# Kernel tuning notes

Measured on AMD Instinct MI355X. Metric: run time of the kernel, lower is better.

The kernel has to match this reference:

```python
import jax, jax.numpy as jnp
import numpy as np

EDGES = np.array([[0,13],[0,1],[0,4],[0,10],[0,7],[13,14],[14,15],[15,16],[1,2],[2,3],
                  [3,17],[4,5],[5,6],[6,18],[10,11],[11,12],[12,19],[7,8],[8,9],[9,20]])
N = 21
EPS = 1e-5


def _build_adj():
    # adj_mx_from_edges: symmetric binary adjacency + self-loops, row-normalized (D^-1 (A+I))
    A = np.zeros((N, N), np.float32)
    A[EDGES[:, 0], EDGES[:, 1]] = 1.0
    A = np.maximum(A, A.T)
    A = A + np.eye(N, dtype=np.float32)
    A = A / A.sum(1, keepdims=True)
    return A


def setup_inputs() -> dict:
    key = jax.random.key(0)
    ks = jax.random.split(key, 10)
    B, C, H, W = 64, 256, 64, 64
    s = 0.05
    return {
        "feature_s": jax.random.normal(ks[0], (B, C, H, W), jnp.float32),
        "target_s": jax.random.uniform(ks[1], (B, N, H, W), jnp.float32),
        "adj": jnp.asarray(_build_adj()),
        "bn_gamma": jnp.ones((N,), jnp.float32),
        "bn_beta": jnp.zeros((N,), jnp.float32),
        "gru_wx": s * jax.random.normal(ks[2], (256, 768), jnp.float32),
        "gru_wh": s * jax.random.normal(ks[3], (256, 768), jnp.float32),
        "gru_bx": jnp.zeros((768,), jnp.float32),
        "gru_bh": jnp.zeros((768,), jnp.float32),
        "w_g1": s * jax.random.normal(ks[4], (2, 256, 256), jnp.float32),
        "b_g1": jnp.zeros((256,), jnp.float32),
        "w_g2": s * jax.random.normal(ks[5], (2, 256, 256), jnp.float32),
        "b_g2": jnp.zeros((256,), jnp.float32),
        "w_out": s * jax.random.normal(ks[6], (2, 256, 3), jnp.float32),
        "b_out": jnp.zeros((3,), jnp.float32),
    }


def _batchnorm1d(x, gamma, beta):
    # x: [B, 21, C]; BatchNorm1d over channel dim 21 (stats over batch and length)
    mean = jnp.mean(x, axis=(0, 2), keepdims=True)
    var = jnp.var(x, axis=(0, 2), keepdims=True)
    xn = (x - mean) * jax.lax.rsqrt(var + EPS)
    return xn * gamma[None, :, None] + beta[None, :, None]


def _gru(x, wx, wh, bx, bh):
    # standard GRU scanned over the 21-joint axis; x: [B, N, 256] -> [B, N, 256]
    B, n, Hd = x.shape
    xg = jnp.einsum('bnc,ch->bnh', x, wx) + bx  # [B, N, 3H]

    def step(h, xg_t):
        hg = h @ wh + bh
        r = jax.nn.sigmoid(xg_t[..., :Hd] + hg[..., :Hd])
        z = jax.nn.sigmoid(xg_t[..., Hd:2 * Hd] + hg[..., Hd:2 * Hd])
        ncand = jnp.tanh(xg_t[..., 2 * Hd:] + r * hg[..., 2 * Hd:])
        h_new = (1.0 - z) * ncand + z * h
        return h_new, h_new

    h0 = jnp.zeros((B, Hd), x.dtype)
    _, ys = jax.lax.scan(step, h0, jnp.swapaxes(xg, 0, 1))
    return jnp.swapaxes(ys, 0, 1)


def _laplacian(adj):
    # normalized Laplacian L = I - D^{-1/2} A D^{-1/2}
    d = adj.sum(-1)
    dinv = jnp.where(d > 0, jax.lax.rsqrt(jnp.where(d > 0, d, 1.0)), 0.0)
    return jnp.eye(N, dtype=adj.dtype) - dinv[:, None] * adj * dinv[None, :]


def _chebconv(x, L, w, b):
    # K=2 Chebyshev conv: T0 = I, T1 = L ->  x @ W0 + (L x) @ W1 + b
    return jnp.einsum('bnc,co->bno', x, w[0]) + jnp.einsum('nm,bmc,co->bno', L, x, w[1]) + b


def reference(feature_s, target_s, adj, bn_gamma, bn_beta,
              gru_wx, gru_wh, gru_bx, gru_bh,
              w_g1, b_g1, w_g2, b_g2, w_out, b_out):
    B, C, H, W = feature_s.shape
    # batched correlation: [B, 21, HW] x [B, HW, C] -> [B, 21, C]
    q = jnp.einsum('bjp,bcp->bjc',
                   target_s.reshape(B, N, H * W),
                   feature_s.reshape(B, C, H * W))
    q = _batchnorm1d(q, bn_gamma, bn_beta)
    q = jnp.where(q > 0, q, 0.1 * q)  # LeakyReLU(0.1)
    q = _gru(q, gru_wx, gru_wh, gru_bx, gru_bh)
    # _ResChebGC: two graph convs with ReLU + residual (dropout = identity in eval)
    L = _laplacian(adj)
    h = jax.nn.relu(_chebconv(q, L, w_g1, b_g1))
    h = jax.nn.relu(_chebconv(h, L, w_g2, b_g2))
    x = q + h
    return _chebconv(x, L, w_out, b_out)  # [B, 21, 3]
```

## Files before the change

### kernel.cpp

```cpp
#include <hip/hip_runtime.h>
#include <cstdint>

#define B   64
#define NJ  21
#define CHN 256
#define HW  4096
#define G3  768
#define KSTEP 64

typedef _Float16 f16x8 __attribute__((ext_vector_type(8)));
typedef float    f32x4 __attribute__((ext_vector_type(4)));
typedef _Float16 f16x2 __attribute__((ext_vector_type(2)));
typedef __fp16   fp16x2v __attribute__((ext_vector_type(2)));
union PKU { fp16x2v h; unsigned u; };
union HU { unsigned u; f16x2 h; };

static __device__ inline unsigned pack_f16(float a, float b){
  HU u; u.h.x = (_Float16)a; u.h.y = (_Float16)b; return u.u;
}

__global__ __launch_bounds__(64) void k_lap(const float* __restrict__ adj, float* __restrict__ L){
  __shared__ float dinv[NJ];
  int t = threadIdx.x;
  if (t < NJ){
    float s = 0.f;
    for (int j=0;j<NJ;j++) s += adj[t*NJ+j];
    dinv[t] = s > 0.f ? 1.f/sqrtf(s) : 0.f;
  }
  __syncthreads();
  for (int idx=t; idx<NJ*NJ; idx+=64){
    int i = idx/NJ, j = idx%NJ;
    L[idx] = (i==j ? 1.f : 0.f) - dinv[i]*adj[idx]*dinv[j];
  }
}

__global__ __launch_bounds__(256,2) void k_corr2(const float* __restrict__ T,
    const float* __restrict__ F, _Float16* __restrict__ P){
  int bid = blockIdx.x;
  int nb = bid & 3, b = (bid>>2)&63, kb = bid>>8;
  int t = threadIdx.x;
  int w = t>>6, l = t&63;
  __shared__ __align__(16) unsigned short At[2][32*KSTEP];
  __shared__ __align__(16) unsigned short Bt[2][64*KSTEP];

  for (int i=t; i<704; i+=256){
    int bi = (i>=352) ? 1 : 0; int r2 = i - bi*352;
    int r = 21 + (r2>>5); int kk = r2 & 31;
    *(unsigned*)((char*)&At[bi][0] + r*128 + kk*4) = 0u;
  }

  bool isF = (t < 128);
  bool isT = (t >= 128) && (t < 170);
  const float4* gp = nullptr; int srow = 0, shalf = 0;
  if (isF){
    srow = t>>1; shalf = t&1;
    gp = (const float4*)(F + ((size_t)b*CHN + nb*64 + srow)*HW + (size_t)kb*2048) + shalf*8;
  } else if (isT){
    int tt = t-128; srow = tt>>1; shalf = tt&1;
    gp = (const float4*)(T + ((size_t)b*NJ + srow)*HW + (size_t)kb*2048) + shalf*8;
  }
  float4 ld[8];
  if (gp){
    #pragma unroll
    for (int i=0;i<8;i++) ld[i] = gp[i];
  }

  f32x4 acc0 = {0.f,0.f,0.f,0.f}, acc1 = {0.f,0.f,0.f,0.f};
  int arow0 = (l&15);
  int brow  = w*16 + (l&15);
  int kbyt  = (l>>4)*16;

  for (int s=0; s<32; ++s){
    int bi = s & 1;
    if (gp){
      unsigned short* tile = isF ? &Bt[bi][0] : &At[bi][0];
      #pragma unroll
      for (int i=0;i<8;i++){
        PKU p0, p1;
        p0.h = __builtin_amdgcn_cvt_pkrtz(ld[i].x, ld[i].y);
        p1.h = __builtin_amdgcn_cvt_pkrtz(ld[i].z, ld[i].w);
        int addr = (srow*128 + shalf*64 + i*8) ^ ((srow&7)<<4);
        uint2 v; v.x = p0.u; v.y = p1.u;
        *(uint2*)((char*)tile + addr) = v;
      }
      if (s < 31){
        const float4* gn = gp + (size_t)(s+1)*16;
        #pragma unroll
        for (int i=0;i<8;i++) ld[i] = gn[i];
      }
    }
    __syncthreads();
    #pragma unroll
    for (int kc=0;kc<2;kc++){
      int kb2 = kc*64 + kbyt;
      int ab0 = ((arow0)*128      + kb2) ^ ((arow0&7)<<4);
      int ab1 = ((arow0+16)*128   + kb2) ^ ((arow0&7)<<4);
      int bb  = ((brow)*128       + kb2) ^ ((brow&7)<<4);
      f16x8 a0 = *(const f16x8*)((const char*)&At[bi][0] + ab0);
      f16x8 a1 = *(const f16x8*)((const char*)&At[bi][0] + ab1);
      f16x8 bf = *(const f16x8*)((const char*)&Bt[bi][0] + bb);
      acc0 = __builtin_amdgcn_mfma_f32_16x16x32_f16(a0, bf, acc0, 0, 0, 0);
      acc1 = __builtin_amdgcn_mfma_f32_16x16x32_f16(a1, bf, acc1, 0, 0, 0);
    }
    __syncthreads();
  }

  int cbase = nb*64 + w*16 + (l&15);
  #pragma unroll
  for (int r=0;r<4;r++){
    int row0 = (l>>4)*4 + r;
    if (row0 < 21)
      P[(((size_t)kb*64 + b)*21 + row0)*256 + cbase] = (_Float16)acc0[r];
    int row1 = row0 + 16;
    if (row1 < 21)
      P[(((size_t)kb*64 + b)*21 + row1)*256 + cbase] = (_Float16)acc1[r];
  }
}

__global__ __launch_bounds__(256) void k_stats(const _Float16* __restrict__ P,
    float* __restrict__ q, float* __restrict__ stats){
  int j = blockIdx.x, t = threadIdx.x;
  float s = 0.f, ss = 0.f;
  for (int b=0;b<B;b++){
    size_t i0 = ((size_t)b*21 + j)*256 + t;
    float v = (float)P[i0] + (float)P[(size_t)64*21*256 + i0];
    q[((size_t)b*NJ + j)*CHN + t] = v;
    s += v; ss += v*v;
  }
  #pragma unroll
  for (int o=32;o>0;o>>=1){ s += __shfl_down(s,o); ss += __shfl_down(ss,o); }
  __shared__ float sb[4], ssb[4];
  int wid = t>>6;
  if ((t&63)==0){ sb[wid]=s; ssb[wid]=ss; }
  __syncthreads();
  if (t==0){
    float S  = sb[0]+sb[1]+sb[2]+sb[3];
    float SS = ssb[0]+ssb[1]+ssb[2]+ssb[3];
    float mean = S * (1.f/16384.f);
    float var  = SS * (1.f/16384.f) - mean*mean;
    stats[j]      = mean;
    stats[NJ + j] = 1.f/sqrtf(var + 1e-5f);
  }
}

__global__ __launch_bounds__(256) void k_xg(const float* __restrict__ q,
    const float* __restrict__ stats, const float* __restrict__ gamma, const float* __restrict__ beta,
    const float* __restrict__ wx, const float* __restrict__ bx, float* __restrict__ xg){
  int b = blockIdx.x/3, sl = blockIdx.x%3;
  int t = threadIdx.x;
  int col = sl*256 + t;
  __shared__ float xn[NJ][CHN];
  for (int idx=t; idx<NJ*CHN; idx+=256){
    int j = idx >> 8;
    float v = (q[(size_t)b*NJ*CHN + idx] - stats[j]) * stats[NJ+j];
    v = v * gamma[j] + beta[j];
    xn[j][idx & 255] = v > 0.f ? v : 0.1f*v;
  }
  __syncthreads();
  float acc[NJ];
  #pragma unroll
  for (int j=0;j<NJ;j++) acc[j]=0.f;
  for (int c=0;c<CHN;c++){
    float wv = wx[(size_t)c*G3 + col];
    #pragma unroll
    for (int j=0;j<NJ;j++) acc[j] += xn[j][c]*wv;
  }
  float bv = bx[col];
  #pragma unroll
  for (int j=0;j<NJ;j++) xg[((size_t)b*NJ+j)*G3 + col] = acc[j] + bv;
}

__global__ __launch_bounds__(256) void k_pack(const float* __restrict__ wh, unsigned* __restrict__ whp){
  int idx = blockIdx.x*256 + threadIdx.x;
  int c2 = idx / G3, col = idx % G3;
  float w0 = wh[(size_t)(2*c2)*G3 + col];
  float w1 = wh[(size_t)(2*c2+1)*G3 + col];
  whp[idx] = pack_f16(w0, w1);
}

__global__ __launch_bounds__(768,3) void k_gru(const unsigned* __restrict__ whp,
    const float* __restrict__ bh, const float* __restrict__ xg, float* __restrict__ gout){
  int b = blockIdx.x;
  int col = threadIdx.x;
  int l = col & 63;
  __shared__ float hf[256];
  __shared__ float lr[256], lz[256];
  float bhv = bh[col];
  if (col < 256) hf[col] = 0.f;
  unsigned hv0 = 0u, hv1 = 0u;
  float xv_next = xg[((size_t)b*NJ + 0)*G3 + col];
  __syncthreads();
  for (int step=0; step<NJ; ++step){
    float xvc = xv_next;
    if (step < NJ-1) xv_next = xg[((size_t)b*NJ + step+1)*G3 + col];
    float a0 = 0.f, a1 = 0.f;
    #pragma unroll
    for (int c2=0; c2<64; ++c2){
      HU w; w.u = whp[c2*G3 + col];
      HU h; h.u = __builtin_amdgcn_readlane(hv0, c2);
#if __has_builtin(__builtin_amdgcn_fdot2)
      a0 = __builtin_amdgcn_fdot2(w.h, h.h, a0, false);
#else
      a0 += (float)w.h.x*(float)h.h.x + (float)w.h.y*(float)h.h.y;
#endif
    }
    #pragma unroll
    for (int c2=0; c2<64; ++c2){
      HU w; w.u = whp[(64+c2)*G3 + col];
      HU h; h.u = __builtin_amdgcn_readlane(hv1, c2);
#if __has_builtin(__builtin_amdgcn_fdot2)
      a1 = __builtin_amdgcn_fdot2(w.h, h.h, a1, false);
#else
      a1 += (float)w.h.x*(float)h.h.x + (float)w.h.y*(float)h.h.y;
#endif
    }
    float a = a0 + a1 + bhv;
    if (col < 256)      lr[col]     = 1.f/(1.f+__expf(-(xvc + a)));
    else if (col < 512) lz[col-256] = 1.f/(1.f+__expf(-(xvc + a)));
    __syncthreads();
    if (col >= 512){
      int i = col - 512;
      float nv = tanhf(xvc + lr[i]*a);
      float z  = lz[i];
      float hnew = (1.f - z)*nv + z*hf[i];
      gout[((size_t)b*NJ + step)*CHN + i] = hnew;
      hf[i] = hnew;
    }
    __syncthreads();
    float2 p0 = *(const float2*)&hf[2*l];
    float2 p1 = *(const float2*)&hf[128 + 2*l];
    hv0 = pack_f16(p0.x, p0.y);
    hv1 = pack_f16(p1.x, p1.y);
  }
}

__global__ __launch_bounds__(256) void k_cheb(const float* __restrict__ xin,
    const float* __restrict__ Lm, const float* __restrict__ W,
    const float* __restrict__ bvec, float* __restrict__ out){
  int b = blockIdx.x >> 2, oq = blockIdx.x & 3;
  int t = threadIdx.x;
  int ol = t & 63, ck = t >> 6;
  __shared__ float xs[NJ][CHN];
  __shared__ float lx[NJ][CHN];
  __shared__ float part[4][64][NJ];
  for (int idx=t; idx<NJ*CHN; idx+=256) xs[idx>>8][idx&255] = xin[(size_t)b*NJ*CHN + idx];
  __syncthreads();
  for (int idx=t; idx<NJ*CHN; idx+=256){
    int j = idx>>8, c = idx&255;
    float sacc = 0.f;
    #pragma unroll
    for (int m=0;m<NJ;m++) sacc += Lm[j*NJ+m]*xs[m][c];
    lx[j][c] = sacc;
  }
  __syncthreads();
  int o = oq*64 + ol;
  float acc[NJ];
  #pragma unroll
  for (int j=0;j<NJ;j++) acc[j]=0.f;
  const float* W0 = W;
  const float* W1 = W + CHN*CHN;
  for (int cc=0; cc<64; ++cc){
    int c = ck*64 + cc;
    float w0 = W0[(size_t)c*CHN + o];
    float w1 = W1[(size_t)c*CHN + o];
    #pragma unroll
    for (int j=0;j<NJ;j++){ acc[j] += xs[j][c]*w0; acc[j] += lx[j][c]*w1; }
  }
  #pragma unroll
  for (int j=0;j<NJ;j++) part[ck][ol][j] = acc[j];
  __syncthreads();
  for (int idx=t; idx<64*NJ; idx+=256){
    int o2 = idx & 63, j = idx >> 6;
    float s2 = part[0][o2][j]+part[1][o2][j]+part[2][o2][j]+part[3][o2][j] + bvec[oq*64+o2];
    s2 = s2 > 0.f ? s2 : 0.f;
    out[(size_t)b*NJ*CHN + j*CHN + oq*64 + o2] = s2;
  }
}

__global__ __launch_bounds__(64) void k_out(const float* __restrict__ gq, const float* __restrict__ h2,
    const float* __restrict__ Lm, const float* __restrict__ W, const float* __restrict__ bvec,
    float* __restrict__ out){
  int b = blockIdx.x, t = threadIdx.x;
  __shared__ float xs[NJ][CHN];
  __shared__ float lx[NJ][CHN];
  for (int idx=t; idx<NJ*CHN; idx+=64)
    xs[idx>>8][idx&255] = gq[(size_t)b*NJ*CHN+idx] + h2[(size_t)b*NJ*CHN+idx];
  __syncthreads();
  for (int idx=t; idx<NJ*CHN; idx+=64){
    int j = idx>>8, c = idx&255;
    float s = 0.f;
    #pragma unroll
    for (int m=0;m<NJ;m++) s += Lm[j*NJ+m]*xs[m][c];
    lx[j][c] = s;
  }
  __syncthreads();
  if (t < 63){
    int j = t/3, o = t%3;
    float acc = bvec[o];
    const float* W0 = W;
    const float* W1 = W + CHN*3;
    for (int c=0;c<CHN;c++){
      acc += xs[j][c]*W0[c*3+o];
      acc += lx[j][c]*W1[c*3+o];
    }
    out[(size_t)b*63 + t] = acc;
  }
}

extern "C" void kernel_launch(void* const* d_in, const int* in_sizes, int n_in,
                              void* d_out, int out_size, void* d_ws, size_t ws_size,
                              hipStream_t stream){
  const float* feat  = (const float*)d_in[0];
  const float* targ  = (const float*)d_in[1];
  const float* adj   = (const float*)d_in[2];
  const float* gamma = (const float*)d_in[3];
  const float* beta  = (const float*)d_in[4];
  const float* wx    = (const float*)d_in[5];
  const float* wh    = (const float*)d_in[6];
  const float* bx    = (const float*)d_in[7];
  const float* bh    = (const float*)d_in[8];
  const float* wg1   = (const float*)d_in[9];
  const float* bg1   = (const float*)d_in[10];
  const float* wg2   = (const float*)d_in[11];
  const float* bg2   = (const float*)d_in[12];
  const float* wout  = (const float*)d_in[13];
  const float* bout  = (const float*)d_in[14];

  float* ws   = (float*)d_ws;
  float* q     = ws + 0;
  float* stats = ws + 344064;
  float* Lw    = ws + 344128;
  float* xgw   = ws + 344576;
  float* gout  = ws + 1376768;
  float* h1    = ws + 1720832;
  float* h2b   = ws + 2064896;
  _Float16* P = (_Float16*)(ws + 344576);
  unsigned* whp = (unsigned*)h1;

  k_lap  <<<1,    64, 0, stream>>>(adj, Lw);
  k_pack <<<384, 256, 0, stream>>>(wh, whp);
  k_corr2<<<512, 256, 0, stream>>>(targ, feat, P);
  k_stats<<<21,  256, 0, stream>>>(P, q, stats);
  k_xg   <<<192, 256, 0, stream>>>(q, stats, gamma, beta, wx, bx, xgw);
  k_gru  <<<64,  768, 0, stream>>>(whp, bh, xgw, gout);
  k_cheb <<<256, 256, 0, stream>>>(gout, Lw, wg1, bg1, h1);
  k_cheb <<<256, 256, 0, stream>>>(h1,   Lw, wg2, bg2, h2b);
  k_out  <<<64,   64, 0, stream>>>(gout, h2b, Lw, wout, bout, (float*)d_out);
}
```

Measured before the change: 262.1 us.

## Split correlation K four ways, cache GRU weights in registers, trim barriers

The correlation kernel now splits the 4096-long reduction into four chunks over 1024 blocks instead of two chunks over 512, to raise occupancy. It stores tiles with 16-byte LDS writes and uses one barrier per step instead of two. The stats kernel sums four partials. The GRU recurrent weights are repacked per column so each thread keeps its 128 packed weights in registers across all 21 steps instead of reloading them from global memory each step. That register cost may cause spills or limit occupancy, and dropping the trailing barrier relies on double buffering to avoid races.

Measured after the change: 280.2 us. 6.9% more time.

```diff
diff --git a/kernel.cpp b/kernel.cpp
--- a/kernel.cpp
+++ b/kernel.cpp
@@ -6,7 +6,6 @@
 #define CHN 256
 #define HW  4096
 #define G3  768
-#define KSTEP 64
 
 typedef _Float16 f16x8 __attribute__((ext_vector_type(8)));
 typedef float    f32x4 __attribute__((ext_vector_type(4)));
@@ -34,14 +33,14 @@
   }
 }
 
-__global__ __launch_bounds__(256,2) void k_corr2(const float* __restrict__ T,
+__global__ __launch_bounds__(256,4) void k_corr3(const float* __restrict__ T,
     const float* __restrict__ F, _Float16* __restrict__ P){
   int bid = blockIdx.x;
   int nb = bid & 3, b = (bid>>2)&63, kb = bid>>8;
   int t = threadIdx.x;
   int w = t>>6, l = t&63;
-  __shared__ __align__(16) unsigned short At[2][32*KSTEP];
-  __shared__ __align__(16) unsigned short Bt[2][64*KSTEP];
+  __shared__ __align__(16) unsigned short At[2][32*64];
+  __shared__ __align__(16) unsigned short Bt[2][64*64];
 
   for (int i=t; i<704; i+=256){
     int bi = (i>=352) ? 1 : 0; int r2 = i - bi*352;
@@ -54,10 +53,10 @@
   const float4* gp = nullptr; int srow = 0, shalf = 0;
   if (isF){
     srow = t>>1; shalf = t&1;
-    gp = (const float4*)(F + ((size_t)b*CHN + nb*64 + srow)*HW + (size_t)kb*2048) + shalf*8;
+    gp = (const float4*)(F + ((size_t)b*CHN + nb*64 + srow)*HW + (size_t)kb*1024) + shalf*8;
   } else if (isT){
     int tt = t-128; srow = tt>>1; shalf = tt&1;
-    gp = (const float4*)(T + ((size_t)b*NJ + srow)*HW + (size_t)kb*2048) + shalf*8;
+    gp = (const float4*)(T + ((size_t)b*NJ + srow)*HW + (size_t)kb*1024) + shalf*8;
   }
   float4 ld[8];
   if (gp){
@@ -70,39 +69,40 @@
   int brow  = w*16 + (l&15);
   int kbyt  = (l>>4)*16;
 
-  for (int s=0; s<32; ++s){
+  for (int s=0; s<16; ++s){
     int bi = s & 1;
     if (gp){
       unsigned short* tile = isF ? &Bt[bi][0] : &At[bi][0];
       #pragma unroll
-      for (int i=0;i<8;i++){
-        PKU p0, p1;
-        p0.h = __builtin_amdgcn_cvt_pkrtz(ld[i].x, ld[i].y);
-        p1.h = __builtin_amdgcn_cvt_pkrtz(ld[i].z, ld[i].w);
-        int addr = (srow*128 + shalf*64 + i*8) ^ ((srow&7)<<4);
-        uint2 v; v.x = p0.u; v.y = p1.u;
-        *(uint2*)((char*)tile + addr) = v;
+      for (int q=0;q<4;q++){
+        PKU p0, p1, p2, p3;
+        p0.h = __builtin_amdgcn_cvt_pkrtz(ld[2*q].x,   ld[2*q].y);
+        p1.h = __builtin_amdgcn_cvt_pkrtz(ld[2*q].z,   ld[2*q].w);
+        p2.h = __builtin_amdgcn_cvt_pkrtz(ld[2*q+1].x, ld[2*q+1].y);
+        p3.h = __builtin_amdgcn_cvt_pkrtz(ld[2*q+1].z, ld[2*q+1].w);
+        int addr = (srow*128 + shalf*64 + q*16) ^ ((srow&7)<<4);
+        uint4 v; v.x = p0.u; v.y = p1.u; v.z = p2.u; v.w = p3.u;
+        *(uint4*)((char*)tile + addr) = v;
       }
-      if (s < 31){
+      if (s < 15){
         const float4* gn = gp + (size_t)(s+1)*16;
         #pragma unroll
         for (int i=0;i<8;i++) ld[i] = gn[i];
       }
     }
-    __syncthreads();
+    asm volatile("s_waitcnt lgkmcnt(0)\n\ts_barrier" ::: "memory");
     #pragma unroll
     for (int kc=0;kc<2;kc++){
       int kb2 = kc*64 + kbyt;
-      int ab0 = ((arow0)*128      + kb2) ^ ((arow0&7)<<4);
-      int ab1 = ((arow0+16)*128   + kb2) ^ ((arow0&7)<<4);
-      int bb  = ((brow)*128       + kb2) ^ ((brow&7)<<4);
+      int ab0 = ((arow0)*128    + kb2) ^ ((arow0&7)<<4);
+      int ab1 = ((arow0+16)*128 + kb2) ^ ((arow0&7)<<4);
+      int bb  = ((brow)*128     + kb2) ^ ((brow&7)<<4);
       f16x8 a0 = *(const f16x8*)((const char*)&At[bi][0] + ab0);
       f16x8 a1 = *(const f16x8*)((const char*)&At[bi][0] + ab1);
       f16x8 bf = *(const f16x8*)((const char*)&Bt[bi][0] + bb);
       acc0 = __builtin_amdgcn_mfma_f32_16x16x32_f16(a0, bf, acc0, 0, 0, 0);
       acc1 = __builtin_amdgcn_mfma_f32_16x16x32_f16(a1, bf, acc1, 0, 0, 0);
     }
-    __syncthreads();
   }
 
   int cbase = nb*64 + w*16 + (l&15);
@@ -120,10 +120,12 @@
 __global__ __launch_bounds__(256) void k_stats(const _Float16* __restrict__ P,
     float* __restrict__ q, float* __restrict__ stats){
   int j = blockIdx.x, t = threadIdx.x;
+  const size_t KSTRIDE = (size_t)64*21*256;
   float s = 0.f, ss = 0.f;
   for (int b=0;b<B;b++){
     size_t i0 = ((size_t)b*21 + j)*256 + t;
-    float v = (float)P[i0] + (float)P[(size_t)64*21*256 + i0];
+    float v = (float)P[i0] + (float)P[KSTRIDE + i0]
+            + (float)P[2*KSTRIDE + i0] + (float)P[3*KSTRIDE + i0];
     q[((size_t)b*NJ + j)*CHN + t] = v;
     s += v; ss += v*v;
   }
@@ -170,21 +172,25 @@
   for (int j=0;j<NJ;j++) xg[((size_t)b*NJ+j)*G3 + col] = acc[j] + bv;
 }
 
-__global__ __launch_bounds__(256) void k_pack(const float* __restrict__ wh, unsigned* __restrict__ whp){
+__global__ __launch_bounds__(256) void k_pack2(const float* __restrict__ wh, unsigned* __restrict__ whp2){
   int idx = blockIdx.x*256 + threadIdx.x;
-  int c2 = idx / G3, col = idx % G3;
+  int col = idx >> 7, c2 = idx & 127;
   float w0 = wh[(size_t)(2*c2)*G3 + col];
   float w1 = wh[(size_t)(2*c2+1)*G3 + col];
-  whp[idx] = pack_f16(w0, w1);
-}
-
-__global__ __launch_bounds__(768,3) void k_gru(const unsigned* __restrict__ whp,
+  whp2[idx] = pack_f16(w0, w1);
+}
+
+__global__ __launch_bounds__(768,3) void k_gru(const unsigned* __restrict__ whp2,
     const float* __restrict__ bh, const float* __restrict__ xg, float* __restrict__ gout){
   int b = blockIdx.x;
   int col = threadIdx.x;
   int l = col & 63;
   __shared__ float hf[256];
   __shared__ float lr[256], lz[256];
+  uint4 wreg[32];
+  const uint4* wp = (const uint4*)(whp2 + (size_t)col*128);
+  #pragma unroll
+  for (int i=0;i<32;i++) wreg[i] = wp[i];
   float bhv = bh[col];
   if (col < 256) hf[col] = 0.f;
   unsigned hv0 = 0u, hv1 = 0u;
@@ -193,28 +199,25 @@
   for (int step=0; step<NJ; ++step){
     float xvc = xv_next;
     if (step < NJ-1) xv_next = xg[((size_t)b*NJ + step+1)*G3 + col];
-    float a0 = 0.f, a1 = 0.f;
-    #pragma unroll
-    for (int c2=0; c2<64; ++c2){
-      HU w; w.u = whp[c2*G3 + col];
-      HU h; h.u = __builtin_amdgcn_readlane(hv0, c2);
+    float a = 0.f;
+    #pragma unroll
+    for (int i=0;i<32;i++){
+      unsigned w0 = wreg[i].x, w1 = wreg[i].y, w2 = wreg[i].z, w3 = wreg[i].w;
+      int c2 = i*4;
+      HU w, h;
 #if __has_builtin(__builtin_amdgcn_fdot2)
-      a0 = __builtin_amdgcn_fdot2(w.h, h.h, a0, false);
+      w.u=w0; h.u=__builtin_amdgcn_readlane(c2<64?hv0:hv1, c2&63);       a=__builtin_amdgcn_fdot2(w.h,h.h,a,false);
+      w.u=w1; h.u=__builtin_amdgcn_readlane((c2+1)<64?hv0:hv1,(c2+1)&63); a=__builtin_amdgcn_fdot2(w.h,h.h,a,false);
+      w.u=w2; h.u=__builtin_amdgcn_readlane((c2+2)<64?hv0:hv1,(c2+2)&63); a=__builtin_amdgcn_fdot2(w.h,h.h,a,false);
+      w.u=w3; h.u=__builtin_amdgcn_readlane((c2+3)<64?hv0:hv1,(c2+3)&63); a=__builtin_amdgcn_fdot2(w.h,h.h,a,false);
 #else
-      a0 += (float)w.h.x*(float)h.h.x + (float)w.h.y*(float)h.h.y;
+      w.u=w0; h.u=__builtin_amdgcn_readlane(c2<64?hv0:hv1, c2&63);       a+=(float)w.h.x*(float)h.h.x+(float)w.h.y*(float)h.h.y;
+      w.u=w1; h.u=__builtin_amdgcn_readlane((c2+1)<64?hv0:hv1,(c2+1)&63); a+=(float)w.h.x*(float)h.h.x+(float)w.h.y*(float)h.h.y;
+      w.u=w2; h.u=__builtin_amdgcn_readlane((c2+2)<64?hv0:hv1,(c2+2)&63); a+=(float)w.h.x*(float)h.h.x+(float)w.h.y*(float)h.h.y;
+      w.u=w3; h.u=__builtin_amdgcn_readlane((c2+3)<64?hv0:hv1,(c2+3)&63); a+=(float)w.h.x*(float)h.h.x+(float)w.h.y*(float)h.h.y;
 #endif
     }
-    #pragma unroll
-    for (int c2=0; c2<64; ++c2){
-      HU w; w.u = whp[(64+c2)*G3 + col];
-      HU h; h.u = __builtin_amdgcn_readlane(hv1, c2);
-#if __has_builtin(__builtin_amdgcn_fdot2)
-      a1 = __builtin_amdgcn_fdot2(w.h, h.h, a1, false);
-#else
-      a1 += (float)w.h.x*(float)h.h.x + (float)w.h.y*(float)h.h.y;
-#endif
-    }
-    float a = a0 + a1 + bhv;
+    a += bhv;
     if (col < 256)      lr[col]     = 1.f/(1.f+__expf(-(xvc + a)));
     else if (col < 512) lz[col-256] = 1.f/(1.f+__expf(-(xvc + a)));
     __syncthreads();
@@ -328,21 +331,21 @@
 
   float* ws   = (float*)d_ws;
   float* q     = ws + 0;
-  float* stats = ws + 344064;
-  float* Lw    = ws + 344128;
-  float* xgw   = ws + 344576;
-  float* gout  = ws + 1376768;
-  float* h1    = ws + 1720832;
-  float* h2b   = ws + 2064896;
-  _Float16* P = (_Float16*)(ws + 344576);
-  unsigned* whp = (unsigned*)h1;
+  float* stats = ws + 400000;
+  float* Lw    = ws + 400128;
+  float* xgw   = ws + 500000;
+  float* gout  = ws + 1600000;
+  float* h1    = ws + 2000000;
+  float* h2b   = ws + 2400000;
+  unsigned* whp2 = (unsigned*)(ws + 2800000);
+  _Float16* P  = (_Float16*)(ws + 3000000);
 
   k_lap  <<<1,    64, 0, stream>>>(adj, Lw);
-  k_pack <<<384, 256, 0, stream>>>(wh, whp);
-  k_corr2<<<512, 256, 0, stream>>>(targ, feat, P);
+  k_pack2<<<384, 256, 0, stream>>>(wh, whp2);
+  k_corr3<<<1024,256, 0, stream>>>(targ, feat, P);
   k_stats<<<21,  256, 0, stream>>>(P, q, stats);
   k_xg   <<<192, 256, 0, stream>>>(q, stats, gamma, beta, wx, bx, xgw);
-  k_gru  <<<64,  768, 0, stream>>>(whp, bh, xgw, gout);
+  k_gru  <<<64,  768, 0, stream>>>(whp2, bh, xgw, gout);
   k_cheb <<<256, 256, 0, stream>>>(gout, Lw, wg1, bg1, h1);
   k_cheb <<<256, 256, 0, stream>>>(h1,   Lw, wg2, bg2, h2b);
   k_out  <<<64,   64, 0, stream>>>(gout, h2b, Lw, wout, bout, (float*)d_out);
```
